# Kernel optimization log

Measured on AMD Instinct MI355X. Metric: run time of the kernel, lower is better.

The kernel has to match this reference:

```python
import jax, jax.numpy as jnp
import numpy as np

B, NP, K = 8, 512, 64   # graphs, points per graph, knn neighbors
N = B * NP              # total nodes
EPS = 1e-5


def knn_edges(pos):
    """knn_graph(pos, k=K, batch, loop=True): edges (src=j neighbor, dst=i)."""
    p = pos.reshape(B, NP, 3)
    d2 = jnp.sum((p[:, :, None, :] - p[:, None, :, :]) ** 2, axis=-1)  # [B,NP,NP]
    _, idx = jax.lax.top_k(-d2, K)  # [B,NP,K] nearest (self included, d2=0)
    off = (jnp.arange(B, dtype=jnp.int32) * NP)[:, None, None]
    src = (idx.astype(jnp.int32) + off).reshape(-1)
    dst = jnp.broadcast_to(jnp.arange(NP, dtype=jnp.int32)[None, :, None] + off,
                           (B, NP, K)).reshape(-1)
    return src, dst


def graph_norm(x, batch, w, b, ms):
    """PyG GraphNorm: per-graph mean/std with learnable mean scale."""
    cnt = jax.ops.segment_sum(jnp.ones((x.shape[0], 1), x.dtype), batch, B)
    mean = jax.ops.segment_sum(x, batch, B) / cnt
    out = x - mean[batch] * ms
    var = jax.ops.segment_sum(out * out, batch, B) / cnt
    return w * out / jnp.sqrt(var + EPS)[batch] + b


def pointnet_layer(h, pos, src, dst, w1, b1, w2, b2):
    """message = MLP(concat(h_j, pos_j - pos_i)); aggregate = scatter-max over dst."""
    m = jnp.concatenate([h[src], pos[src] - pos[dst]], axis=-1)  # [E, Cin+3]
    m = jax.nn.relu(m @ w1 + b1) @ w2 + b2                        # [E, Cout]
    return jax.ops.segment_max(m, dst, N)


def _forward(batch, pos,
             gn1_w, gn1_b, gn1_ms, gn2_w, gn2_b, gn2_ms, gn3_w, gn3_b, gn3_ms,
             gn4_w, gn4_b, gn4_ms, gn5_w, gn5_b, gn5_ms, gn6_w, gn6_b, gn6_ms,
             c1_w1, c1_b1, c1_w2, c1_b2, c2_w1, c2_b1, c2_w2, c2_b2,
             c3_w1, c3_b1, c3_w2, c3_b2, c4_w1, c4_b1, c4_w2, c4_b2,
             c5_w1, c5_b1, c5_w2, c5_b2, cls_w, cls_b):
    src, dst = knn_edges(pos)
    h = graph_norm(pos, batch, gn1_w, gn1_b, gn1_ms)
    h = pointnet_layer(h, pos, src, dst, c1_w1, c1_b1, c1_w2, c1_b2)
    h = jax.nn.relu(graph_norm(h, batch, gn2_w, gn2_b, gn2_ms))
    h = pointnet_layer(h, pos, src, dst, c2_w1, c2_b1, c2_w2, c2_b2)
    h = jax.nn.relu(graph_norm(h, batch, gn3_w, gn3_b, gn3_ms))
    h = pointnet_layer(h, pos, src, dst, c3_w1, c3_b1, c3_w2, c3_b2)
    h = jax.nn.relu(graph_norm(h, batch, gn4_w, gn4_b, gn4_ms))
    h = pointnet_layer(h, pos, src, dst, c4_w1, c4_b1, c4_w2, c4_b2)
    h = jax.nn.relu(graph_norm(h, batch, gn5_w, gn5_b, gn5_ms))
    h = pointnet_layer(h, pos, src, dst, c5_w1, c5_b1, c5_w2, c5_b2)
    h = jax.nn.relu(graph_norm(h, batch, gn6_w, gn6_b, gn6_ms))
    return h @ cls_w + cls_b  # [N, 14]


def setup_inputs() -> dict:
    key = jax.random.key(0)
    ks = iter(jax.random.split(key, 40))
    inp = {}
    inp["pos"] = jax.random.normal(next(ks), (N, 3), jnp.float32)
    inp["batch"] = jnp.repeat(jnp.arange(B, dtype=jnp.int32), NP)
    for i, c in enumerate([3, 64, 128, 256, 512, 512], 1):
        inp[f"gn{i}_w"] = jnp.ones((c,), jnp.float32)
        inp[f"gn{i}_b"] = jnp.zeros((c,), jnp.float32)
        inp[f"gn{i}_ms"] = jnp.ones((c,), jnp.float32)
    for i, (ci, co) in enumerate([(3, 64), (64, 128), (128, 256), (256, 512), (512, 512)], 1):
        fin = ci + 3
        inp[f"c{i}_w1"] = jax.random.normal(next(ks), (fin, co), jnp.float32) / np.sqrt(fin).astype(np.float32)
        inp[f"c{i}_b1"] = jnp.zeros((co,), jnp.float32)
        inp[f"c{i}_w2"] = jax.random.normal(next(ks), (co, co), jnp.float32) / np.sqrt(co).astype(np.float32)
        inp[f"c{i}_b2"] = jnp.zeros((co,), jnp.float32)
    inp["cls_w"] = jax.random.normal(next(ks), (512, 14), jnp.float32) / np.float32(np.sqrt(512))
    inp["cls_b"] = jnp.zeros((14,), jnp.float32)
    return inp


def reference(pos, batch,
              gn1_w, gn1_b, gn1_ms, gn2_w, gn2_b, gn2_ms, gn3_w, gn3_b, gn3_ms,
              gn4_w, gn4_b, gn4_ms, gn5_w, gn5_b, gn5_ms, gn6_w, gn6_b, gn6_ms,
              c1_w1, c1_b1, c1_w2, c1_b2, c2_w1, c2_b1, c2_w2, c2_b2,
              c3_w1, c3_b1, c3_w2, c3_b2, c4_w1, c4_b1, c4_w2, c4_b2,
              c5_w1, c5_b1, c5_w2, c5_b2, cls_w, cls_b):
    return _forward(batch, pos,
                    gn1_w, gn1_b, gn1_ms, gn2_w, gn2_b, gn2_ms, gn3_w, gn3_b, gn3_ms,
                    gn4_w, gn4_b, gn4_ms, gn5_w, gn5_b, gn5_ms, gn6_w, gn6_b, gn6_ms,
                    c1_w1, c1_b1, c1_w2, c1_b2, c2_w1, c2_b1, c2_w2, c2_b2,
                    c3_w1, c3_b1, c3_w2, c3_b2, c4_w1, c4_b1, c4_w2, c4_b2,
                    c5_w1, c5_b1, c5_w2, c5_b2, cls_w, cls_b)
```

## Files before the change

### kernel.cpp

```cpp
#include <hip/hip_runtime.h>
#include <stdint.h>

#define N_NODES 4096
#define NGRAPH 8
#define NPTS 512
#define KNN 64
#define EPSN 1e-5f

typedef _Float16 f16x8 __attribute__((ext_vector_type(8)));
typedef float f32x4 __attribute__((ext_vector_type(4)));
typedef unsigned long long u64;

__device__ __forceinline__ unsigned short f2h(float f) {
    _Float16 h = (_Float16)f;
    union { _Float16 h; unsigned short u; } cv; cv.h = h;
    return cv.u;
}

__device__ __forceinline__ void w2cv(const float* __restrict__ src, unsigned short* __restrict__ dst,
                                     int off, int lg2c) {
    int C = 1 << lg2c;
    int k = off >> lg2c, n = off & (C - 1);
    int d = ((n >> 4) * (C / 32) + (k >> 5)) * 512 + ((k >> 3) & 3) * 128 + (n & 15) * 8 + (k & 7);
    dst[d] = f2h(src[off]);
}

__global__ __launch_bounds__(64) void setup_kernel(const float* __restrict__ pos, int* __restrict__ knn_out,
                                                   const float* __restrict__ wa, const float* __restrict__ wb,
                                                   const float* __restrict__ wc, const float* __restrict__ wd,
                                                   const float* __restrict__ we,
                                                   unsigned short* __restrict__ oa, unsigned short* __restrict__ ob,
                                                   unsigned short* __restrict__ oc, unsigned short* __restrict__ od,
                                                   unsigned short* __restrict__ oe,
                                                   float* __restrict__ statz,
                                                   const float* __restrict__ ms1, const float* __restrict__ gw1,
                                                   float* __restrict__ Aa, float* __restrict__ Sa) {
#pragma clang fp contract(off)
    __shared__ float px[NPTS], py[NPTS], pz[NPTS];
    __shared__ u64 keys[NPTS];
    int bid = blockIdx.x;
    int tid = threadIdx.x;
    int gidx = bid * 64 + tid;
    for (int idx = gidx; idx < 40960; idx += 262144) statz[idx] = 0.f;
    for (int idx = gidx; idx < 610304; idx += 262144) {
        if (idx < 4096)        w2cv(wa, oa, idx, 6);
        else if (idx < 20480)  w2cv(wb, ob, idx - 4096, 7);
        else if (idx < 86016)  w2cv(wc, oc, idx - 20480, 8);
        else if (idx < 348160) w2cv(wd, od, idx - 86016, 9);
        else                   w2cv(we, oe, idx - 348160, 9);
    }
    if (bid < 24) {
        int g = bid / 3, ch = bid - g * 3;
        float s1 = 0.f, s2 = 0.f;
        for (int n = tid; n < NPTS; n += 64) {
            float v = pos[(g * NPTS + n) * 3 + ch];
            s1 += v; s2 += v * v;
        }
        #pragma unroll
        for (int off = 32; off; off >>= 1) { s1 += __shfl_xor(s1, off); s2 += __shfl_xor(s2, off); }
        if (tid == 0) {
            float mean = s1 * (1.f / NPTS);
            float av = mean * ms1[ch];
            float var = s2 * (1.f / NPTS) - 2.f * av * mean + av * av;
            Aa[g * 3 + ch] = av;
            Sa[g * 3 + ch] = gw1[ch] / sqrtf(var + EPSN);
        }
    }
    int b = bid >> 9;
    int il = bid & (NPTS - 1);
    for (int n = tid; n < NPTS; n += 64) {
        int base = (b * NPTS + n) * 3;
        px[n] = pos[base]; py[n] = pos[base + 1]; pz[n] = pos[base + 2];
    }
    __syncthreads();
    float xi = px[il], yi = py[il], zi = pz[il];
    for (int n = tid; n < NPTS; n += 64) {
        float dx = px[n] - xi, dy = py[n] - yi, dz = pz[n] - zi;
        float d2 = dx * dx;
        d2 = d2 + dy * dy;
        d2 = d2 + dz * dz;
        keys[n] = (((u64)__float_as_uint(d2)) << 32) | (unsigned)n;
    }
    __syncthreads();
    for (int k2 = 2; k2 <= NPTS; k2 <<= 1) {
        for (int j = k2 >> 1; j > 0; j >>= 1) {
            #pragma unroll 4
            for (int p = 0; p < 4; ++p) {
                int pid = tid + p * 64;
                int t = ((pid & ~(j - 1)) << 1) | (pid & (j - 1));
                int ixj = t | j;
                u64 a = keys[t], c = keys[ixj];
                bool up = ((t & k2) == 0);
                if ((a > c) == up) { keys[t] = c; keys[ixj] = a; }
            }
            __syncthreads();
        }
    }
    int j0 = (int)(keys[tid] & 0xffffffffu);
    knn_out[(size_t)(b * NPTS + il) * KNN + tid] = b * NPTS + j0;
}

template<int CIN, int C, int RELU, int RAW>
__global__ __launch_bounds__(C) void node_kernel(const float* __restrict__ y, const float* __restrict__ pos,
                                                 const float* __restrict__ p1, const float* __restrict__ p2,
                                                 const float* __restrict__ ms, const float* __restrict__ gw,
                                                 const float* __restrict__ bnp,
                                                 const float* __restrict__ w1, const float* __restrict__ b1,
                                                 float* __restrict__ U, float* __restrict__ P) {
    constexpr int ROWS = 16;
    constexpr int KC = 64;
    constexpr int LDH = KC + 4;
    __shared__ float hs[ROWS][LDH];
    __shared__ float As_[CIN > 0 ? CIN : 1], Ss_[CIN > 0 ? CIN : 1];
    const int c = threadIdx.x;
    const int n0 = blockIdx.x * ROWS;
    const int b = n0 >> 9;
    if (RAW) {
        for (int ch = c; ch < CIN; ch += C) {
            float s1 = p1[b * CIN + ch], s2 = p2[b * CIN + ch];
            float mean = s1 * (1.f / NPTS);
            float a = mean * ms[ch];
            float var = s2 * (1.f / NPTS) - 2.f * a * mean + a * a;
            As_[ch] = a;
            Ss_[ch] = gw[ch] / sqrtf(var + EPSN);
        }
    }
    float acc[ROWS];
    #pragma unroll
    for (int r = 0; r < ROWS; ++r) acc[r] = 0.f;
    constexpr int NCHUNK = (CIN + KC - 1) / KC;
    #pragma unroll 1
    for (int s = 0; s < NCHUNK; ++s) {
        const int k0 = s * KC;
        const int kc = (CIN - k0 < KC) ? (CIN - k0) : KC;
        __syncthreads();
        for (int idx = c; idx < ROWS * kc; idx += C) {
            int r = idx / kc, k = idx - r * kc;
            int ch = k0 + k;
            float a = RAW ? As_[ch] : p1[b * CIN + ch];
            float sf = RAW ? Ss_[ch] : p2[b * CIN + ch];
            float v = (y[(size_t)(n0 + r) * CIN + ch] - a) * sf + bnp[ch];
            if (RELU) v = fmaxf(v, 0.f);
            hs[r][k] = v;
        }
        __syncthreads();
        int k = 0;
        for (; k + 4 <= kc; k += 4) {
            float w0 = w1[(size_t)(k0 + k) * C + c];
            float w1v = w1[(size_t)(k0 + k + 1) * C + c];
            float w2v = w1[(size_t)(k0 + k + 2) * C + c];
            float w3v = w1[(size_t)(k0 + k + 3) * C + c];
            #pragma unroll
            for (int r = 0; r < ROWS; ++r) {
                f32x4 hv = *(const f32x4*)&hs[r][k];
                acc[r] = fmaf(hv[0], w0, acc[r]);
                acc[r] = fmaf(hv[1], w1v, acc[r]);
                acc[r] = fmaf(hv[2], w2v, acc[r]);
                acc[r] = fmaf(hv[3], w3v, acc[r]);
            }
        }
        for (; k < kc; ++k) {
            float wv = w1[(size_t)(k0 + k) * C + c];
            #pragma unroll
            for (int r = 0; r < ROWS; ++r)
                acc[r] = fmaf(hs[r][k], wv, acc[r]);
        }
    }
    float pacc[ROWS];
    #pragma unroll
    for (int r = 0; r < ROWS; ++r) pacc[r] = 0.f;
    #pragma unroll
    for (int e = 0; e < 3; ++e) {
        float wv = w1[(size_t)(CIN + e) * C + c];
        #pragma unroll
        for (int r = 0; r < ROWS; ++r)
            pacc[r] = fmaf(pos[(n0 + r) * 3 + e], wv, pacc[r]);
    }
    float bv = b1[c];
    #pragma unroll
    for (int r = 0; r < ROWS; ++r) {
        U[(size_t)(n0 + r) * C + c] = acc[r] + pacc[r] + bv;
        P[(size_t)(n0 + r) * C + c] = pacc[r];
    }
}

template<int C, int W>
__global__ __launch_bounds__(W * 64, 4) void edge_kernel(const float* __restrict__ U, const float* __restrict__ P,
                                                         const int* __restrict__ knn, const unsigned short* __restrict__ w2t,
                                                         const float* __restrict__ b2, float* __restrict__ Y,
                                                         float* __restrict__ sum1, float* __restrict__ sum2) {
    constexpr int NCT = C / (W * 16);
    constexpr int EPT = 32 / W;
    constexpr int S = C / 32;
    constexpr int LD = 40;
    __shared__ unsigned short Tb[2][64 * LD];
    __shared__ int jn[64];
    __shared__ float Pr[C];
    const int bid = blockIdx.x;
    const int i = ((bid & 7) << 9) | (bid >> 3);
    const int tid = threadIdx.x;
    const int wave = tid >> 6, lane = tid & 63, m = lane & 15, quad = lane >> 4;
    const int cw = wave * (NCT * 16);
    if (tid < 64) jn[tid] = knn[(size_t)i * KNN + tid];
    for (int idx = tid; idx < C; idx += W * 64) Pr[idx] = P[(size_t)i * C + idx];
    f32x4 acc[4][NCT];
    f32x4 zero = {0.f, 0.f, 0.f, 0.f};
    #pragma unroll
    for (int rt = 0; rt < 4; ++rt)
        #pragma unroll
        for (int ct = 0; ct < NCT; ++ct)
            acc[rt][ct] = zero;
    const int rr = tid / W;
    const int c0 = (tid % W) * EPT;
    __syncthreads();
    const float* upr = U + (size_t)jn[rr] * C + c0;
    float4 uf[EPT / 4];
    #pragma unroll
    for (int g = 0; g < EPT / 4; ++g)
        uf[g] = *(const float4*)(upr + g * 4);
    #pragma unroll 2
    for (int s = 0; s < S; ++s) {
        unsigned short* tb = Tb[s & 1];
        if constexpr (EPT == 8) {
            float4 p0 = *(const float4*)&Pr[s * 32 + c0];
            float4 p1 = *(const float4*)&Pr[s * 32 + c0 + 4];
            uint4 pk;
            pk.x = (unsigned)f2h(fmaxf(uf[0].x - p0.x, 0.f)) | ((unsigned)f2h(fmaxf(uf[0].y - p0.y, 0.f)) << 16);
            pk.y = (unsigned)f2h(fmaxf(uf[0].z - p0.z, 0.f)) | ((unsigned)f2h(fmaxf(uf[0].w - p0.w, 0.f)) << 16);
            pk.z = (unsigned)f2h(fmaxf(uf[1].x - p1.x, 0.f)) | ((unsigned)f2h(fmaxf(uf[1].y - p1.y, 0.f)) << 16);
            pk.w = (unsigned)f2h(fmaxf(uf[1].z - p1.z, 0.f)) | ((unsigned)f2h(fmaxf(uf[1].w - p1.w, 0.f)) << 16);
            *(uint4*)&tb[rr * LD + c0] = pk;
        } else {
            float4 p0 = *(const float4*)&Pr[s * 32 + c0];
            uint2 pk;
            pk.x = (unsigned)f2h(fmaxf(uf[0].x - p0.x, 0.f)) | ((unsigned)f2h(fmaxf(uf[0].y - p0.y, 0.f)) << 16);
            pk.y = (unsigned)f2h(fmaxf(uf[0].z - p0.z, 0.f)) | ((unsigned)f2h(fmaxf(uf[0].w - p0.w, 0.f)) << 16);
            *(uint2*)&tb[rr * LD + c0] = pk;
        }
        if (s + 1 < S) {
            #pragma unroll
            for (int g = 0; g < EPT / 4; ++g)
                uf[g] = *(const float4*)(upr + (s + 1) * 32 + g * 4);
        }
        __syncthreads();
        f16x8 a[4];
        #pragma unroll
        for (int rt = 0; rt < 4; ++rt)
            a[rt] = *(const f16x8*)&tb[(rt * 16 + m) * LD + quad * 8];
        #pragma unroll
        for (int ct = 0; ct < NCT; ++ct) {
            const f16x8 bb = *(const f16x8*)(w2t +
                (size_t)(((cw >> 4) + ct) * S + s) * 512 + quad * 128 + m * 8);
            #pragma unroll
            for (int rt = 0; rt < 4; ++rt)
                acc[rt][ct] = __builtin_amdgcn_mfma_f32_16x16x32_f16(a[rt], bb, acc[rt][ct], 0, 0, 0);
        }
    }
    const int gb = i >> 9;
    #pragma unroll
    for (int ct = 0; ct < NCT; ++ct) {
        float vmax = -3.4e38f;
        #pragma unroll
        for (int rt = 0; rt < 4; ++rt) {
            vmax = fmaxf(vmax, acc[rt][ct][0]);
            vmax = fmaxf(vmax, acc[rt][ct][1]);
            vmax = fmaxf(vmax, acc[rt][ct][2]);
            vmax = fmaxf(vmax, acc[rt][ct][3]);
        }
        vmax = fmaxf(vmax, __shfl_xor(vmax, 16));
        vmax = fmaxf(vmax, __shfl_xor(vmax, 32));
        if (quad == 0) {
            int col = cw + ct * 16 + m;
            float val = vmax + b2[col];
            Y[(size_t)i * C + col] = val;
            atomicAdd(&sum1[gb * C + col], val);
            atomicAdd(&sum2[gb * C + col], val * val);
        }
    }
}

__global__ __launch_bounds__(256) void cls_kernel(const float* __restrict__ y, const float* __restrict__ sum1,
                                                  const float* __restrict__ sum2, const float* __restrict__ ms,
                                                  const float* __restrict__ gw, const float* __restrict__ gnb,
                                                  const float* __restrict__ w, const float* __restrict__ bias,
                                                  float* __restrict__ out) {
    __shared__ float wl[512 * 14];
    __shared__ _Float16 hn[16][520];
    __shared__ float As[512], Ss[512];
    int tid = threadIdx.x;
    int n0 = blockIdx.x * 16;
    int b = n0 >> 9;
    for (int ch = tid; ch < 512; ch += 256) {
        float s1 = sum1[b * 512 + ch], s2 = sum2[b * 512 + ch];
        float mean = s1 * (1.f / NPTS);
        float a = mean * ms[ch];
        float var = s2 * (1.f / NPTS) - 2.f * a * mean + a * a;
        As[ch] = a;
        Ss[ch] = gw[ch] / sqrtf(var + EPSN);
    }
    for (int idx = tid; idx < 512 * 14; idx += 256) wl[idx] = w[idx];
    __syncthreads();
    for (int idx = tid; idx < 16 * 512; idx += 256) {
        int r = idx >> 9, k = idx & 511;
        float v = (y[(size_t)(n0 + r) * 512 + k] - As[k]) * Ss[k] + gnb[k];
        hn[r][k] = (_Float16)fmaxf(v, 0.f);
    }
    __syncthreads();
    if (tid < 224) {
        int nl = tid / 14, c = tid - nl * 14;
        float acc = bias[c];
        for (int k = 0; k < 512; ++k)
            acc += (float)hn[nl][k] * wl[k * 14 + c];
        out[(size_t)(n0 + nl) * 14 + c] = acc;
    }
}

extern "C" void kernel_launch(void* const* d_in, const int* in_sizes, int n_in,
                              void* d_out, int out_size, void* d_ws, size_t ws_size,
                              hipStream_t stream) {
    const float* pos = (const float*)d_in[0];
    const float* gnw[6]; const float* gnb[6]; const float* gnms[6];
    for (int i = 0; i < 6; ++i) {
        gnw[i]  = (const float*)d_in[2 + 3 * i];
        gnb[i]  = (const float*)d_in[3 + 3 * i];
        gnms[i] = (const float*)d_in[4 + 3 * i];
    }
    const float* cw1[5]; const float* cb1[5]; const float* cw2[5]; const float* cb2[5];
    for (int i = 0; i < 5; ++i) {
        cw1[i] = (const float*)d_in[20 + 4 * i];
        cb1[i] = (const float*)d_in[21 + 4 * i];
        cw2[i] = (const float*)d_in[22 + 4 * i];
        cb2[i] = (const float*)d_in[23 + 4 * i];
    }
    const float* clsw = (const float*)d_in[40];
    const float* clsb = (const float*)d_in[41];
    float* out = (float*)d_out;

    char* ws = (char*)d_ws;
    int* knn             = (int*)(ws + 0);
    float* U             = (float*)(ws + 1048576);
    float* P             = (float*)(ws + 9437184);
    float* y             = (float*)(ws + 26214400);
    float* Aa            = (float*)(ws + 34603008);
    float* Sa            = (float*)(ws + 34619392);
    unsigned short* w2t0 = (unsigned short*)(ws + 34635776);
    unsigned short* w2t1 = (unsigned short*)(ws + 34643968);
    unsigned short* w2t2 = (unsigned short*)(ws + 34676736);
    unsigned short* w2t3 = (unsigned short*)(ws + 34807808);
    unsigned short* w2t4 = (unsigned short*)(ws + 35332096);
    float* acc           = (float*)(ws + 35856384);
    float* s1l[5]; float* s2l[5];
    for (int l = 0; l < 5; ++l) { s1l[l] = acc + l * 8192; s2l[l] = s1l[l] + 4096; }

    setup_kernel<<<N_NODES, 64, 0, stream>>>(pos, knn, cw2[0], cw2[1], cw2[2], cw2[3], cw2[4],
                                             w2t0, w2t1, w2t2, w2t3, w2t4, acc,
                                             gnms[0], gnw[0], Aa, Sa);

    node_kernel<3, 64, 0, 0><<<N_NODES / 16, 64, 0, stream>>>(pos, pos, Aa, Sa, gnms[0], gnw[0], gnb[0], cw1[0], cb1[0], U, P);
    edge_kernel<64, 4><<<N_NODES, 256, 0, stream>>>(U, P, knn, w2t0, cb2[0], y, s1l[0], s2l[0]);

    node_kernel<64, 128, 1, 1><<<N_NODES / 16, 128, 0, stream>>>(y, pos, s1l[0], s2l[0], gnms[1], gnw[1], gnb[1], cw1[1], cb1[1], U, P);
    edge_kernel<128, 8><<<N_NODES, 512, 0, stream>>>(U, P, knn, w2t1, cb2[1], y, s1l[1], s2l[1]);

    node_kernel<128, 256, 1, 1><<<N_NODES / 16, 256, 0, stream>>>(y, pos, s1l[1], s2l[1], gnms[2], gnw[2], gnb[2], cw1[2], cb1[2], U, P);
    edge_kernel<256, 8><<<N_NODES, 512, 0, stream>>>(U, P, knn, w2t2, cb2[2], y, s1l[2], s2l[2]);

    node_kernel<256, 512, 1, 1><<<N_NODES / 16, 512, 0, stream>>>(y, pos, s1l[2], s2l[2], gnms[3], gnw[3], gnb[3], cw1[3], cb1[3], U, P);
    edge_kernel<512, 8><<<N_NODES, 512, 0, stream>>>(U, P, knn, w2t3, cb2[3], y, s1l[3], s2l[3]);

    node_kernel<512, 512, 1, 1><<<N_NODES / 16, 512, 0, stream>>>(y, pos, s1l[3], s2l[3], gnms[4], gnw[4], gnb[4], cw1[4], cb1[4], U, P);
    edge_kernel<512, 8><<<N_NODES, 512, 0, stream>>>(U, P, knn, w2t4, cb2[4], y, s1l[4], s2l[4]);

    cls_kernel<<<N_NODES / 16, 256, 0, stream>>>(y, s1l[4], s2l[4], gnms[5], gnw[5], gnb[5], clsw, clsb, out);
}
```

Measured before the change: 727.6 us.

## Fuse node and edge stages of last two layers with grid barrier

Replaces the separate node_kernel and edge_kernel launches for layers 4 and 5 with one persistent kernel of 512 blocks. The blocks run the node MLP, meet at a software grid barrier built on an atomic counter, then loop over nodes for the edge MFMA stage and the max aggregation. This removes two kernel launches and the gaps between them. In exchange it relies on all 512 blocks being co-resident, otherwise the barrier deadlocks, and it cuts node-stage parallelism to 256 active blocks. Y is also passed as both input and output, but the barrier orders the reads before the writes.

Result: slower. 1.326 ms (+82.2%).

```diff
diff --git a/kernel.cpp b/kernel.cpp
--- a/kernel.cpp
+++ b/kernel.cpp
@@ -6,6 +6,7 @@
 #define NPTS 512
 #define KNN 64
 #define EPSN 1e-5f
+#define FBLK 512
 
 typedef _Float16 f16x8 __attribute__((ext_vector_type(8)));
 typedef float f32x4 __attribute__((ext_vector_type(4)));
@@ -23,6 +24,19 @@
     int k = off >> lg2c, n = off & (C - 1);
     int d = ((n >> 4) * (C / 32) + (k >> 5)) * 512 + ((k >> 3) & 3) * 128 + (n & 15) * 8 + (k & 7);
     dst[d] = f2h(src[off]);
+}
+
+__device__ __forceinline__ void gridbar(u64* cnt) {
+    __syncthreads();
+    if (threadIdx.x == 0) {
+        __threadfence();
+        u64 old = __hip_atomic_fetch_add(cnt, 1ull, __ATOMIC_ACQ_REL, __HIP_MEMORY_SCOPE_AGENT);
+        u64 target = (old / FBLK + 1) * FBLK;
+        while (__hip_atomic_load(cnt, __ATOMIC_ACQUIRE, __HIP_MEMORY_SCOPE_AGENT) < target)
+            __builtin_amdgcn_s_sleep(2);
+        __threadfence();
+    }
+    __syncthreads();
 }
 
 __global__ __launch_bounds__(64) void setup_kernel(const float* __restrict__ pos, int* __restrict__ knn_out,
@@ -279,6 +293,160 @@
     }
 }
 
+template<int CIN>
+__global__ __launch_bounds__(512, 4) void fused_kernel(const float* __restrict__ y, const float* __restrict__ pos,
+                                                       const float* __restrict__ p1, const float* __restrict__ p2,
+                                                       const float* __restrict__ ms, const float* __restrict__ gw,
+                                                       const float* __restrict__ bnp,
+                                                       const float* __restrict__ w1, const float* __restrict__ b1,
+                                                       float* __restrict__ U, float* __restrict__ P,
+                                                       const int* __restrict__ knn, const unsigned short* __restrict__ w2t,
+                                                       const float* __restrict__ b2, float* __restrict__ Y,
+                                                       float* __restrict__ sum1, float* __restrict__ sum2,
+                                                       u64* __restrict__ bar) {
+    constexpr int C = 512;
+    constexpr int ROWS = 16;
+    constexpr int KC = 64;
+    constexpr int LDH = KC + 4;
+    constexpr int NCT = 4, S = 16, LD = 40;
+    __shared__ union {
+        struct { float hs[ROWS][LDH]; float As_[512], Ss_[512]; } n;
+        struct { unsigned short Tb[2][64 * LD]; int jn[64]; float Pr[C]; } e;
+    } sm;
+    const int bid = blockIdx.x;
+    const int tid = threadIdx.x;
+
+    if (bid < N_NODES / ROWS) {
+        const int c = tid;
+        const int n0 = bid * ROWS;
+        const int b = n0 >> 9;
+        for (int ch = c; ch < CIN; ch += 512) {
+            float s1 = p1[b * CIN + ch], s2 = p2[b * CIN + ch];
+            float mean = s1 * (1.f / NPTS);
+            float a = mean * ms[ch];
+            float var = s2 * (1.f / NPTS) - 2.f * a * mean + a * a;
+            sm.n.As_[ch] = a;
+            sm.n.Ss_[ch] = gw[ch] / sqrtf(var + EPSN);
+        }
+        float acc[ROWS];
+        #pragma unroll
+        for (int r = 0; r < ROWS; ++r) acc[r] = 0.f;
+        constexpr int NCHUNK = (CIN + KC - 1) / KC;
+        #pragma unroll 1
+        for (int s = 0; s < NCHUNK; ++s) {
+            const int k0 = s * KC;
+            const int kc = (CIN - k0 < KC) ? (CIN - k0) : KC;
+            __syncthreads();
+            for (int idx = c; idx < ROWS * kc; idx += 512) {
+                int r = idx / kc, k = idx - r * kc;
+                int ch = k0 + k;
+                float v = (y[(size_t)(n0 + r) * CIN + ch] - sm.n.As_[ch]) * sm.n.Ss_[ch] + bnp[ch];
+                sm.n.hs[r][k] = fmaxf(v, 0.f);
+            }
+            __syncthreads();
+            int k = 0;
+            for (; k + 4 <= kc; k += 4) {
+                float w0 = w1[(size_t)(k0 + k) * C + c];
+                float w1v = w1[(size_t)(k0 + k + 1) * C + c];
+                float w2v = w1[(size_t)(k0 + k + 2) * C + c];
+                float w3v = w1[(size_t)(k0 + k + 3) * C + c];
+                #pragma unroll
+                for (int r = 0; r < ROWS; ++r) {
+                    f32x4 hv = *(const f32x4*)&sm.n.hs[r][k];
+                    acc[r] = fmaf(hv[0], w0, acc[r]);
+                    acc[r] = fmaf(hv[1], w1v, acc[r]);
+                    acc[r] = fmaf(hv[2], w2v, acc[r]);
+                    acc[r] = fmaf(hv[3], w3v, acc[r]);
+                }
+            }
+        }
+        float pacc[ROWS];
+        #pragma unroll
+        for (int r = 0; r < ROWS; ++r) pacc[r] = 0.f;
+        #pragma unroll
+        for (int e = 0; e < 3; ++e) {
+            float wv = w1[(size_t)(CIN + e) * C + c];
+            #pragma unroll
+            for (int r = 0; r < ROWS; ++r)
+                pacc[r] = fmaf(pos[(n0 + r) * 3 + e], wv, pacc[r]);
+        }
+        float bv = b1[c];
+        #pragma unroll
+        for (int r = 0; r < ROWS; ++r) {
+            U[(size_t)(n0 + r) * C + c] = acc[r] + pacc[r] + bv;
+            P[(size_t)(n0 + r) * C + c] = pacc[r];
+        }
+    }
+    gridbar(bar);
+
+    const int wave = tid >> 6, lane = tid & 63, m = lane & 15, quad = lane >> 4;
+    const int cw = wave * (NCT * 16);
+    const int rr = tid >> 3;
+    const int c0 = (tid & 7) * 4;
+    #pragma unroll 1
+    for (int v = bid; v < N_NODES; v += FBLK) {
+        const int i = ((v & 7) << 9) | (v >> 3);
+        if (tid < 64) sm.e.jn[tid] = knn[(size_t)i * KNN + tid];
+        for (int idx = tid; idx < C; idx += 512) sm.e.Pr[idx] = P[(size_t)i * C + idx];
+        f32x4 acc[4][NCT];
+        f32x4 zero = {0.f, 0.f, 0.f, 0.f};
+        #pragma unroll
+        for (int rt = 0; rt < 4; ++rt)
+            #pragma unroll
+            for (int ct = 0; ct < NCT; ++ct)
+                acc[rt][ct] = zero;
+        __syncthreads();
+        const float* upr = U + (size_t)sm.e.jn[rr] * C + c0;
+        float4 uf = *(const float4*)upr;
+        #pragma unroll 2
+        for (int s = 0; s < S; ++s) {
+            unsigned short* tb = sm.e.Tb[s & 1];
+            float4 p0 = *(const float4*)&sm.e.Pr[s * 32 + c0];
+            uint2 pk;
+            pk.x = (unsigned)f2h(fmaxf(uf.x - p0.x, 0.f)) | ((unsigned)f2h(fmaxf(uf.y - p0.y, 0.f)) << 16);
+            pk.y = (unsigned)f2h(fmaxf(uf.z - p0.z, 0.f)) | ((unsigned)f2h(fmaxf(uf.w - p0.w, 0.f)) << 16);
+            *(uint2*)&tb[rr * LD + c0] = pk;
+            if (s + 1 < S)
+                uf = *(const float4*)(upr + (s + 1) * 32);
+            __syncthreads();
+            f16x8 a[4];
+            #pragma unroll
+            for (int rt = 0; rt < 4; ++rt)
+                a[rt] = *(const f16x8*)&tb[(rt * 16 + m) * LD + quad * 8];
+            #pragma unroll
+            for (int ct = 0; ct < NCT; ++ct) {
+                const f16x8 bb = *(const f16x8*)(w2t +
+                    (size_t)(((cw >> 4) + ct) * S + s) * 512 + quad * 128 + m * 8);
+                #pragma unroll
+                for (int rt = 0; rt < 4; ++rt)
+                    acc[rt][ct] = __builtin_amdgcn_mfma_f32_16x16x32_f16(a[rt], bb, acc[rt][ct], 0, 0, 0);
+            }
+        }
+        const int gb = i >> 9;
+        #pragma unroll
+        for (int ct = 0; ct < NCT; ++ct) {
+            float vmax = -3.4e38f;
+            #pragma unroll
+            for (int rt = 0; rt < 4; ++rt) {
+                vmax = fmaxf(vmax, acc[rt][ct][0]);
+                vmax = fmaxf(vmax, acc[rt][ct][1]);
+                vmax = fmaxf(vmax, acc[rt][ct][2]);
+                vmax = fmaxf(vmax, acc[rt][ct][3]);
+            }
+            vmax = fmaxf(vmax, __shfl_xor(vmax, 16));
+            vmax = fmaxf(vmax, __shfl_xor(vmax, 32));
+            if (quad == 0) {
+                int col = cw + ct * 16 + m;
+                float val = vmax + b2[col];
+                Y[(size_t)i * C + col] = val;
+                atomicAdd(&sum1[gb * C + col], val);
+                atomicAdd(&sum2[gb * C + col], val * val);
+            }
+        }
+        __syncthreads();
+    }
+}
+
 __global__ __launch_bounds__(256) void cls_kernel(const float* __restrict__ y, const float* __restrict__ sum1,
                                                   const float* __restrict__ sum2, const float* __restrict__ ms,
                                                   const float* __restrict__ gw, const float* __restrict__ gnb,
@@ -349,8 +517,11 @@
     unsigned short* w2t3 = (unsigned short*)(ws + 34807808);
     unsigned short* w2t4 = (unsigned short*)(ws + 35332096);
     float* acc           = (float*)(ws + 35856384);
+    u64* bar             = (u64*)(ws + 36020224);
     float* s1l[5]; float* s2l[5];
     for (int l = 0; l < 5; ++l) { s1l[l] = acc + l * 8192; s2l[l] = s1l[l] + 4096; }
+
+    hipMemsetAsync((void*)bar, 0, 64, stream);
 
     setup_kernel<<<N_NODES, 64, 0, stream>>>(pos, knn, cw2[0], cw2[1], cw2[2], cw2[3], cw2[4],
                                              w2t0, w2t1, w2t2, w2t3, w2t4, acc,
@@ -365,11 +536,13 @@
     node_kernel<128, 256, 1, 1><<<N_NODES / 16, 256, 0, stream>>>(y, pos, s1l[1], s2l[1], gnms[2], gnw[2], gnb[2], cw1[2], cb1[2], U, P);
     edge_kernel<256, 8><<<N_NODES, 512, 0, stream>>>(U, P, knn, w2t2, cb2[2], y, s1l[2], s2l[2]);
 
-    node_kernel<256, 512, 1, 1><<<N_NODES / 16, 512, 0, stream>>>(y, pos, s1l[2], s2l[2], gnms[3], gnw[3], gnb[3], cw1[3], cb1[3], U, P);
-    edge_kernel<512, 8><<<N_NODES, 512, 0, stream>>>(U, P, knn, w2t3, cb2[3], y, s1l[3], s2l[3]);
-
-    node_kernel<512, 512, 1, 1><<<N_NODES / 16, 512, 0, stream>>>(y, pos, s1l[3], s2l[3], gnms[4], gnw[4], gnb[4], cw1[4], cb1[4], U, P);
-    edge_kernel<512, 8><<<N_NODES, 512, 0, stream>>>(U, P, knn, w2t4, cb2[4], y, s1l[4], s2l[4]);
+    fused_kernel<256><<<FBLK, 512, 0, stream>>>(y, pos, s1l[2], s2l[2], gnms[3], gnw[3], gnb[3],
+                                                cw1[3], cb1[3], U, P, knn, w2t3, cb2[3], y,
+                                                s1l[3], s2l[3], bar);
+
+    fused_kernel<512><<<FBLK, 512, 0, stream>>>(y, pos, s1l[3], s2l[3], gnms[4], gnw[4], gnb[4],
+                                                cw1[4], cb1[4], U, P, knn, w2t4, cb2[4], y,
+                                                s1l[4], s2l[4], bar);
 
     cls_kernel<<<N_NODES / 16, 256, 0, stream>>>(y, s1l[4], s2l[4], gnms[5], gnw[5], gnb[5], clsw, clsb, out);
 }
```
